# Performance work log

Measured on AMD Instinct MI355X. Metric: run time of the kernel, lower is better.

The kernel has to match this reference:

```python
import jax, jax.numpy as jnp
import numpy as np

N, D_IN, D_OUT = 4096, 1024, 1024
DROPOUT_RATE = 0.1


def setup_inputs() -> dict:
    key = jax.random.key(0)
    kx, kq, kk, kv = jax.random.split(key, 4)
    s = 1.0 / np.sqrt(D_IN)
    return {
        "x": jax.random.normal(kx, (N, D_IN), dtype=jnp.float32),
        "wq": jax.random.normal(kq, (D_OUT, D_IN), dtype=jnp.float32) * s,
        "wk": jax.random.normal(kk, (D_OUT, D_IN), dtype=jnp.float32) * s,
        "wv": jax.random.normal(kv, (D_OUT, D_IN), dtype=jnp.float32) * s,
    }


def reference(x, wq, wk, wv):
    # torch Linear: y = x @ W.T  (no bias since qkv_bias=False)
    q = x @ wq.T                      # [N, d_out]
    k = x @ wk.T
    v = x @ wv.T
    scores = q @ k.T                  # [N, N]
    n = scores.shape[0]
    causal = jnp.tril(jnp.ones((n, n), dtype=bool))  # keep lower triangle
    masked = jnp.where(causal, scores, -jnp.inf)
    scale = k.shape[-1] ** 0.5
    weights = jax.nn.softmax(masked / scale, axis=-1)
    # dropout (train mode), fixed key for determinism
    keep = jax.random.bernoulli(jax.random.key(42), 1.0 - DROPOUT_RATE, weights.shape)
    weights = jnp.where(keep, weights / (1.0 - DROPOUT_RATE), 0.0)
    return weights @ v                # [N, d_out]
```

## Files before the change

### kernel.cpp

```cpp
#include <hip/hip_runtime.h>
#include <hip/hip_fp16.h>

typedef __attribute__((ext_vector_type(8))) _Float16 f16x8;
typedef __attribute__((ext_vector_type(4))) float f32x4;

typedef const __attribute__((address_space(1))) void gas_void;
typedef __attribute__((address_space(3))) void las_void;
typedef __attribute__((address_space(3))) const __half las_chalf;

__device__ __forceinline__ f16x8 ldsr(const __half* p) {
    f16x8 r;
    asm volatile("ds_read_b128 %0, %1" : "=v"(r) : "v"((las_chalf*)p));
    return r;
}

__global__ __launch_bounds__(256) void cast_all_k(const float* __restrict__ x,
                                                  const float* __restrict__ wq,
                                                  const float* __restrict__ wk,
                                                  const float* __restrict__ wv,
                                                  __half* __restrict__ xb,
                                                  __half* __restrict__ wqkv) {
    const int b = blockIdx.x;
    const float* src;
    __half* dst;
    size_t i;
    if (b < 2048) {
        src = x; dst = xb;
        i = ((size_t)b * 256 + threadIdx.x) * 8;
    } else {
        const int w = (b - 2048) >> 9;
        src = w == 0 ? wq : (w == 1 ? wk : wv);
        dst = wqkv + (size_t)w * 1048576;
        i = (((size_t)((b - 2048) & 511)) * 256 + threadIdx.x) * 8;
    }
    float4 a = *(const float4*)(src + i);
    float4 c = *(const float4*)(src + i + 4);
    __half2 h[4] = { __floats2half2_rn(a.x, a.y), __floats2half2_rn(a.z, a.w),
                     __floats2half2_rn(c.x, c.y), __floats2half2_rn(c.z, c.w) };
    *(int4*)(dst + i) = *(int4*)h;
}

template <int MODE>
__global__ __launch_bounds__(512, 2)
void gemm256(const __half* __restrict__ pA, const __half* __restrict__ pB,
             void* __restrict__ pC, void* __restrict__ pC2,
             __half* __restrict__ PH1, __half* __restrict__ PH2,
             __half* __restrict__ PH3, __half* __restrict__ PH4,
             const float* __restrict__ Lr) {
    constexpr int LD = (MODE == 0) ? 1024 : (MODE == 1 ? 2048 : 4096);

    int bi, bj, c = 0, k_lo = 0, NT = 16;
    bool isVT = false;
    if constexpr (MODE == 0) {
        const int id = blockIdx.x;
        const int sw = (id & 7) * 24 + (id >> 3);
        if (sw < 128) { bi = sw >> 3; bj = sw & 7; }
        else          { int s2 = sw - 128; bi = s2 >> 4; bj = s2 & 15; isVT = true; }
    } else if constexpr (MODE == 1) {
        const int id = blockIdx.x;
        const int sw = (id & 7) * 17 + (id >> 3);
        int b = (int)((sqrtf(8.0f * sw + 1.0f) - 1.0f) * 0.5f);
        while ((b + 1) * (b + 2) / 2 <= sw) ++b;
        while (b * (b + 1) / 2 > sw) --b;
        bi = b; bj = sw - b * (b + 1) / 2;
    } else {
        const int id = blockIdx.x;
        const int xcd = id & 7;
        const int sw = (xcd < 4 ? xcd * 25 : 100 + (xcd - 4) * 24) + (id >> 3);
        bj = sw / 49;
        int x = sw - 49 * bj;
        int nch = 1;
        for (bi = 0; bi < 16; ++bi) {
            nch = (4 * (bi + 1) + 12) / 13;
            if (x < nch) { c = x; break; }
            x -= nch;
        }
        const int full = 4 * (bi + 1);
        k_lo = c * 13;
        NT = min(full - k_lo, 13);
    }

    const __half* A = pA;
    const __half* B = pB;
    if constexpr (MODE == 0) {
        if (isVT) { A = pB + 2097152; B = pA; }
    }

    const int brow = bi * 256, bcol = bj * 256;
    const int tid = threadIdx.x;
    const int lane = tid & 63, wid = tid >> 6;
    const int wm = wid >> 2, wn = wid & 3;
    const int lane15 = lane & 15;
    const int kxor = (lane & 7) << 3;
    const int g16 = (lane >> 4) << 3;

    extern __shared__ __half smem[];

    const int srow = (wid << 3) + (lane >> 3);
    const int scol = ((lane & 7) ^ ((lane >> 3) & 7)) << 3;

    auto stage_half = [&](const __half* G, int growbase, int kt, int buf, int mat, int half) {
        const __half* src = G + (size_t)(growbase + half * 128 + srow) * LD + kt * 64 + scol;
        __half* dst = &smem[buf * 32768 + mat * 16384 + (half * 128 + (wid << 3)) * 64];
        __builtin_amdgcn_global_load_lds((gas_void*)src, (las_void*)dst, 16, 0, 0);
        __builtin_amdgcn_global_load_lds((gas_void*)(src + (size_t)64 * LD),
                                         (las_void*)(dst + 64 * 64), 16, 0, 0);
    };

    f32x4 acc[8][4] = {};
    f16x8 bfrag[2][4];

    stage_half(B, bcol, k_lo, 0, 1, 0);
    stage_half(B, bcol, k_lo, 0, 1, 1);
    stage_half(A, brow, k_lo, 0, 0, 0);
    stage_half(A, brow, k_lo, 0, 0, 1);
    if (NT > 1) {
        stage_half(B, bcol, k_lo + 1, 1, 1, 0);
        stage_half(B, bcol, k_lo + 1, 1, 1, 1);
    }

    for (int Tr = 0; Tr < NT; ++Tr) {
        const int Ta = k_lo + Tr;
        const int buf = Tr & 1;
        const __half* Abase = &smem[buf * 32768 + (wm * 128 + lane15) * 64];
        const __half* Bbase = &smem[buf * 32768 + 16384 + (wn * 64 + lane15) * 64];

        if (Tr < NT - 1) asm volatile("s_waitcnt vmcnt(4)" ::: "memory");
        else             asm volatile("s_waitcnt vmcnt(0)" ::: "memory");
        __builtin_amdgcn_s_barrier();

        {
#pragma unroll
            for (int kk = 0; kk < 2; ++kk)
#pragma unroll
                for (int n = 0; n < 4; ++n)
                    bfrag[kk][n] = ldsr(Bbase + (n * 16) * 64 + ((kk * 32 + g16) ^ kxor));
            f16x8 af[2][2];
#pragma unroll
            for (int mi = 0; mi < 2; ++mi)
#pragma unroll
                for (int kk = 0; kk < 2; ++kk)
                    af[mi][kk] = ldsr(Abase + (mi * 16) * 64 + ((kk * 32 + g16) ^ kxor));
            if (Tr + 1 < NT) stage_half(A, brow, Ta + 1, buf ^ 1, 0, 0);
            asm volatile("s_waitcnt lgkmcnt(0)" ::: "memory");
            __builtin_amdgcn_sched_barrier(0);
            __builtin_amdgcn_s_setprio(1);
#pragma unroll
            for (int mi = 0; mi < 2; ++mi)
#pragma unroll
                for (int n = 0; n < 4; ++n)
#pragma unroll
                    for (int kk = 0; kk < 2; ++kk)
                        acc[mi][n] = __builtin_amdgcn_mfma_f32_16x16x32_f16(
                            af[mi][kk], bfrag[kk][n], acc[mi][n], 0, 0, 0);
            __builtin_amdgcn_s_setprio(0);
            __builtin_amdgcn_s_barrier();
        }

#pragma unroll
        for (int p = 1; p < 4; ++p) {
            f16x8 af[2][2];
#pragma unroll
            for (int mi = 0; mi < 2; ++mi)
#pragma unroll
                for (int kk = 0; kk < 2; ++kk)
                    af[mi][kk] = ldsr(Abase + ((2 * p + mi) * 16) * 64 + ((kk * 32 + g16) ^ kxor));
            if (p == 1)      { if (Tr + 1 < NT) stage_half(A, brow, Ta + 1, buf ^ 1, 0, 1); }
            else if (p == 2) { if (Tr + 2 < NT) stage_half(B, bcol, Ta + 2, buf, 1, 0); }
            else             { if (Tr + 2 < NT) stage_half(B, bcol, Ta + 2, buf, 1, 1); }
            asm volatile("s_waitcnt lgkmcnt(0)" ::: "memory");
            __builtin_amdgcn_sched_barrier(0);
            __builtin_amdgcn_s_setprio(1);
#pragma unroll
            for (int mi = 0; mi < 2; ++mi)
#pragma unroll
                for (int n = 0; n < 4; ++n)
#pragma unroll
                    for (int kk = 0; kk < 2; ++kk)
                        acc[2 * p + mi][n] = __builtin_amdgcn_mfma_f32_16x16x32_f16(
                            af[mi][kk], bfrag[kk][n], acc[2 * p + mi][n], 0, 0, 0);
            __builtin_amdgcn_s_setprio(0);
            __builtin_amdgcn_s_barrier();
        }
    }

    const int r0 = (lane >> 4) << 2;
    if constexpr (MODE == 2) {
        if (c == 0) {
            float* Ct = (float*)pC;
            const bool doScale = (4 * (bi + 1) <= 13);
#pragma unroll
            for (int m = 0; m < 8; ++m)
#pragma unroll
                for (int r = 0; r < 4; ++r) {
                    const int row = brow + wm * 128 + m * 16 + r0 + r;
                    const float inv = doScale ? 1.0f / (0.9f * Lr[row]) : 1.0f;
#pragma unroll
                    for (int n = 0; n < 4; ++n) {
                        const int col = bcol + wn * 64 + n * 16 + lane15;
                        Ct[(size_t)row * 1024 + col] = acc[m][n][r] * inv;
                    }
                }
        } else {
            __half* Ph = (c == 1) ? PH1 : (c == 2 ? PH2 : (c == 3 ? PH3 : PH4));
#pragma unroll
            for (int m = 0; m < 8; ++m)
#pragma unroll
                for (int n = 0; n < 4; ++n) {
                    const int col = bcol + wn * 64 + n * 16 + lane15;
#pragma unroll
                    for (int r = 0; r < 4; ++r) {
                        const int row = brow + wm * 128 + m * 16 + r0 + r;
                        Ph[(size_t)row * 1024 + col] = __float2half(acc[m][n][r]);
                    }
                }
        }
    } else {
        __half* Ct = (__half*)pC;
        int ldc = (MODE == 1) ? 4096 : 2048;
        const float scl = (MODE == 1) ? 0.03125f : 1.0f;
        if constexpr (MODE == 0) {
            if (isVT) { Ct = (__half*)pC2; ldc = 4096; }
        }
#pragma unroll
        for (int m = 0; m < 8; ++m)
#pragma unroll
            for (int n = 0; n < 4; ++n) {
                const int col = bcol + wn * 64 + n * 16 + lane15;
#pragma unroll
                for (int r = 0; r < 4; ++r) {
                    const int row = brow + wm * 128 + m * 16 + r0 + r;
                    Ct[(size_t)row * ldc + col] = __float2half(acc[m][n][r] * scl);
                }
            }
    }
}

__global__ __launch_bounds__(256) void pv_merge_k(float* __restrict__ out,
                                                  const __half* __restrict__ PH1,
                                                  const __half* __restrict__ PH2,
                                                  const __half* __restrict__ PH3,
                                                  const __half* __restrict__ PH4,
                                                  const float* __restrict__ L) {
    const int row = 768 + blockIdx.x;
    const int bi = row >> 8;
    const int nch = (4 * (bi + 1) + 12) / 13;
    const float inv = 1.0f / (0.9f * L[row]);
    const size_t o = (size_t)row * 1024 + threadIdx.x * 4;
    float4 s = *(float4*)(out + o);
    const __half* planes[4] = { PH1, PH2, PH3, PH4 };
#pragma unroll 4
    for (int cc = 1; cc < nch; ++cc) {
        const __half2* p2 = (const __half2*)(planes[cc - 1] + o);
        float2 a = __half22float2(p2[0]);
        float2 b = __half22float2(p2[1]);
        s.x += a.x; s.y += a.y; s.z += b.x; s.w += b.y;
    }
    s.x *= inv; s.y *= inv; s.z *= inv; s.w *= inv;
    *(float4*)(out + o) = s;
}

__device__ __forceinline__ uint32_t rotl32(uint32_t x, int d) { return (x << d) | (x >> (32 - d)); }

__device__ __forceinline__ bool keep_bit(uint32_t flat) {
    uint32_t x0 = 0u;
    uint32_t x1 = flat;
    const uint32_t ks0 = 0u, ks1 = 42u, ks2 = 0u ^ 42u ^ 0x1BD11BDAu;
    x0 += ks0; x1 += ks1;
#define TFR(r) { x0 += x1; x1 = rotl32(x1, r); x1 ^= x0; }
    TFR(13) TFR(15) TFR(26) TFR(6)   x0 += ks1; x1 += ks2 + 1u;
    TFR(17) TFR(29) TFR(16) TFR(24)  x0 += ks2; x1 += ks0 + 2u;
    TFR(13) TFR(15) TFR(26) TFR(6)   x0 += ks0; x1 += ks1 + 3u;
    TFR(17) TFR(29) TFR(16) TFR(24)  x0 += ks1; x1 += ks2 + 4u;
    TFR(13) TFR(15) TFR(26) TFR(6)   x0 += ks2; x1 += ks0 + 5u;
#undef TFR
    uint32_t bits = x0 ^ x1;
    float u = __uint_as_float((bits >> 9) | 0x3f800000u) - 1.0f;
    return u < 0.9f;
}

__global__ __launch_bounds__(256) void softdrop_k(__half* __restrict__ SP,
                                                  float* __restrict__ L, int N) {
    const int i = blockIdx.x;
    const int tid = threadIdx.x;
    const int len = i + 1;
    __half* row = SP + (size_t)i * N;

    float l = 0.f;
    const int len8 = len & ~7;
    for (int j = tid * 8; j < len8; j += 2048) {
        int4 pk = *(const int4*)(row + j);
        const __half* hp = (const __half*)&pk;
        __half o8[8];
        const uint32_t base = (uint32_t)i * 4096u + (uint32_t)j;
#pragma unroll
        for (int q = 0; q < 8; ++q) {
            float e = __expf(__half2float(hp[q]));
            l += e;
            o8[q] = keep_bit(base + q) ? __float2half(e) : __float2half(0.0f);
        }
        *(int4*)(row + j) = *(int4*)o8;
    }
    for (int j = len8 + tid; j < len; j += 256) {
        float e = __expf(__half2float(row[j]));
        l += e;
        row[j] = keep_bit((uint32_t)i * 4096u + (uint32_t)j) ? __float2half(e) : __float2half(0.0f);
    }

    for (int off = 1; off < 64; off <<= 1) l += __shfl_xor(l, off);
    __shared__ float ls[4];
    if ((tid & 63) == 0) ls[tid >> 6] = l;
    __syncthreads();
    if (tid == 0) L[i] = ls[0] + ls[1] + ls[2] + ls[3];

    const int zlim = ((i >> 8) << 8) + 256;
    const int za = (len + 7) & ~7;
    for (int j = len + tid; j < min(za, zlim); j += 256) row[j] = __float2half(0.0f);
    const int4 z = {0, 0, 0, 0};
    for (int j = za + tid * 8; j < zlim; j += 2048) *(int4*)(row + j) = z;
}

extern "C" void kernel_launch(void* const* d_in, const int* in_sizes, int n_in,
                              void* d_out, int out_size, void* d_ws, size_t ws_size,
                              hipStream_t stream) {
    const float* x  = (const float*)d_in[0];
    const float* wq = (const float*)d_in[1];
    const float* wk = (const float*)d_in[2];
    const float* wv = (const float*)d_in[3];
    float* out = (float*)d_out;
    char* ws = (char*)d_ws;

    const int N = 4096;

    __half* xb   = (__half*)(ws + 0);
    __half* wqkv = (__half*)(ws + 8388608);
    __half* QK   = (__half*)(ws + 14680064);
    __half* VT   = (__half*)(ws + 31457280);
    __half* SP   = (__half*)(ws + 48234496);
    float*  Lr   = (float*)(ws + 81788928);
    __half* PH1  = (__half*)(ws + 83886080);
    __half* PH2  = (__half*)(ws + 92274688);
    __half* PH3  = (__half*)(ws + 100663296);
    __half* PH4  = (__half*)(ws + 109051904);

    __half* Q = QK;
    __half* K = QK + 1024;

    auto* g0 = gemm256<0>;
    auto* g1 = gemm256<1>;
    auto* g2 = gemm256<2>;
    (void)hipFuncSetAttribute((const void*)g0, hipFuncAttributeMaxDynamicSharedMemorySize, 131072);
    (void)hipFuncSetAttribute((const void*)g1, hipFuncAttributeMaxDynamicSharedMemorySize, 131072);
    (void)hipFuncSetAttribute((const void*)g2, hipFuncAttributeMaxDynamicSharedMemorySize, 131072);

    cast_all_k<<<3584, 256, 0, stream>>>(x, wq, wk, wv, xb, wqkv);

    g0<<<192, 512, 131072, stream>>>(xb, wqkv, QK, VT, nullptr, nullptr, nullptr, nullptr, nullptr);

    g1<<<136, 512, 131072, stream>>>(Q, K, SP, nullptr, nullptr, nullptr, nullptr, nullptr, nullptr);

    softdrop_k<<<N, 256, 0, stream>>>(SP, Lr, N);

    g2<<<196, 512, 131072, stream>>>(SP, VT, out, nullptr, PH1, PH2, PH3, PH4, Lr);

    pv_merge_k<<<3328, 256, 0, stream>>>(out, PH1, PH2, PH3, PH4, Lr);
}
```

Measured before the change: 139.3 us.

## Precompute dropout bitmask in idle QK^T GEMM blocks and zero diagonal in epilogue

```diff
diff --git a/kernel.cpp b/kernel.cpp
--- a/kernel.cpp
+++ b/kernel.cpp
@@ -12,6 +12,25 @@
     f16x8 r;
     asm volatile("ds_read_b128 %0, %1" : "=v"(r) : "v"((las_chalf*)p));
     return r;
+}
+
+__device__ __forceinline__ uint32_t rotl32(uint32_t x, int d) { return (x << d) | (x >> (32 - d)); }
+
+__device__ __forceinline__ bool keep_bit(uint32_t flat) {
+    uint32_t x0 = 0u;
+    uint32_t x1 = flat;
+    const uint32_t ks0 = 0u, ks1 = 42u, ks2 = 0u ^ 42u ^ 0x1BD11BDAu;
+    x0 += ks0; x1 += ks1;
+#define TFR(r) { x0 += x1; x1 = rotl32(x1, r); x1 ^= x0; }
+    TFR(13) TFR(15) TFR(26) TFR(6)   x0 += ks1; x1 += ks2 + 1u;
+    TFR(17) TFR(29) TFR(16) TFR(24)  x0 += ks2; x1 += ks0 + 2u;
+    TFR(13) TFR(15) TFR(26) TFR(6)   x0 += ks0; x1 += ks1 + 3u;
+    TFR(17) TFR(29) TFR(16) TFR(24)  x0 += ks1; x1 += ks2 + 4u;
+    TFR(13) TFR(15) TFR(26) TFR(6)   x0 += ks2; x1 += ks0 + 5u;
+#undef TFR
+    uint32_t bits = x0 ^ x1;
+    float u = __uint_as_float((bits >> 9) | 0x3f800000u) - 1.0f;
+    return u < 0.9f;
 }
 
 __global__ __launch_bounds__(256) void cast_all_k(const float* __restrict__ x,
@@ -46,8 +65,10 @@
              void* __restrict__ pC, void* __restrict__ pC2,
              __half* __restrict__ PH1, __half* __restrict__ PH2,
              __half* __restrict__ PH3, __half* __restrict__ PH4,
-             const float* __restrict__ Lr) {
+             const float* __restrict__ Lr, unsigned char* __restrict__ mask) {
     constexpr int LD = (MODE == 0) ? 1024 : (MODE == 1 ? 2048 : 4096);
+
+    const int tid = threadIdx.x;
 
     int bi, bj, c = 0, k_lo = 0, NT = 16;
     bool isVT = false;
@@ -58,6 +79,28 @@
         else          { int s2 = sw - 128; bi = s2 >> 4; bj = s2 & 15; isVT = true; }
     } else if constexpr (MODE == 1) {
         const int id = blockIdx.x;
+        if (id >= 136) {
+            const int mid = id - 136;
+            for (int pr = mid; pr < 2048; pr += 120) {
+                const int ra = pr;
+                const int rb = 4095 - pr;
+                const int nba = (ra >> 3) + 1;
+                const int nbb = (rb >> 3) + 1;
+                const int tot = nba + nbb;
+                for (int t = tid; t < tot; t += 512) {
+                    int row, b0;
+                    if (t < nba) { row = ra; b0 = t << 3; }
+                    else         { row = rb; b0 = (t - nba) << 3; }
+                    const uint32_t base = (uint32_t)row * 4096u + (uint32_t)b0;
+                    uint32_t bits = 0;
+#pragma unroll
+                    for (int q = 0; q < 8; ++q)
+                        bits |= (keep_bit(base + q) ? 1u : 0u) << q;
+                    mask[(size_t)row * 512 + (b0 >> 3)] = (unsigned char)bits;
+                }
+            }
+            return;
+        }
         const int sw = (id & 7) * 17 + (id >> 3);
         int b = (int)((sqrtf(8.0f * sw + 1.0f) - 1.0f) * 0.5f);
         while ((b + 1) * (b + 2) / 2 <= sw) ++b;
@@ -87,7 +130,6 @@
     }
 
     const int brow = bi * 256, bcol = bj * 256;
-    const int tid = threadIdx.x;
     const int lane = tid & 63, wid = tid >> 6;
     const int wm = wid >> 2, wn = wid & 3;
     const int lane15 = lane & 15;
@@ -222,6 +264,7 @@
         if constexpr (MODE == 0) {
             if (isVT) { Ct = (__half*)pC2; ldc = 4096; }
         }
+        const bool dz = (MODE == 1) && (bi == bj);
 #pragma unroll
         for (int m = 0; m < 8; ++m)
 #pragma unroll
@@ -230,7 +273,9 @@
 #pragma unroll
                 for (int r = 0; r < 4; ++r) {
                     const int row = brow + wm * 128 + m * 16 + r0 + r;
-                    Ct[(size_t)row * ldc + col] = __float2half(acc[m][n][r] * scl);
+                    float v = acc[m][n][r] * scl;
+                    if (dz && col > row) v = 0.0f;
+                    Ct[(size_t)row * ldc + col] = __float2half(v);
                 }
             }
     }
@@ -260,51 +305,35 @@
     *(float4*)(out + o) = s;
 }
 
-__device__ __forceinline__ uint32_t rotl32(uint32_t x, int d) { return (x << d) | (x >> (32 - d)); }
-
-__device__ __forceinline__ bool keep_bit(uint32_t flat) {
-    uint32_t x0 = 0u;
-    uint32_t x1 = flat;
-    const uint32_t ks0 = 0u, ks1 = 42u, ks2 = 0u ^ 42u ^ 0x1BD11BDAu;
-    x0 += ks0; x1 += ks1;
-#define TFR(r) { x0 += x1; x1 = rotl32(x1, r); x1 ^= x0; }
-    TFR(13) TFR(15) TFR(26) TFR(6)   x0 += ks1; x1 += ks2 + 1u;
-    TFR(17) TFR(29) TFR(16) TFR(24)  x0 += ks2; x1 += ks0 + 2u;
-    TFR(13) TFR(15) TFR(26) TFR(6)   x0 += ks0; x1 += ks1 + 3u;
-    TFR(17) TFR(29) TFR(16) TFR(24)  x0 += ks1; x1 += ks2 + 4u;
-    TFR(13) TFR(15) TFR(26) TFR(6)   x0 += ks2; x1 += ks0 + 5u;
-#undef TFR
-    uint32_t bits = x0 ^ x1;
-    float u = __uint_as_float((bits >> 9) | 0x3f800000u) - 1.0f;
-    return u < 0.9f;
-}
-
 __global__ __launch_bounds__(256) void softdrop_k(__half* __restrict__ SP,
-                                                  float* __restrict__ L, int N) {
+                                                  float* __restrict__ L,
+                                                  const unsigned char* __restrict__ mask,
+                                                  int N) {
     const int i = blockIdx.x;
     const int tid = threadIdx.x;
     const int len = i + 1;
     __half* row = SP + (size_t)i * N;
+    const unsigned char* mrow = mask + (size_t)i * 512;
 
     float l = 0.f;
     const int len8 = len & ~7;
     for (int j = tid * 8; j < len8; j += 2048) {
         int4 pk = *(const int4*)(row + j);
         const __half* hp = (const __half*)&pk;
+        const unsigned int mb = mrow[j >> 3];
         __half o8[8];
-        const uint32_t base = (uint32_t)i * 4096u + (uint32_t)j;
 #pragma unroll
         for (int q = 0; q < 8; ++q) {
             float e = __expf(__half2float(hp[q]));
             l += e;
-            o8[q] = keep_bit(base + q) ? __float2half(e) : __float2half(0.0f);
+            o8[q] = ((mb >> q) & 1u) ? __float2half(e) : __float2half(0.0f);
         }
         *(int4*)(row + j) = *(int4*)o8;
     }
     for (int j = len8 + tid; j < len; j += 256) {
         float e = __expf(__half2float(row[j]));
         l += e;
-        row[j] = keep_bit((uint32_t)i * 4096u + (uint32_t)j) ? __float2half(e) : __float2half(0.0f);
+        row[j] = ((mrow[j >> 3] >> (j & 7)) & 1u) ? __float2half(e) : __float2half(0.0f);
     }
 
     for (int off = 1; off < 64; off <<= 1) l += __shfl_xor(l, off);
@@ -312,12 +341,6 @@
     if ((tid & 63) == 0) ls[tid >> 6] = l;
     __syncthreads();
     if (tid == 0) L[i] = ls[0] + ls[1] + ls[2] + ls[3];
-
-    const int zlim = ((i >> 8) << 8) + 256;
-    const int za = (len + 7) & ~7;
-    for (int j = len + tid; j < min(za, zlim); j += 256) row[j] = __float2half(0.0f);
-    const int4 z = {0, 0, 0, 0};
-    for (int j = za + tid * 8; j < zlim; j += 2048) *(int4*)(row + j) = z;
 }
 
 extern "C" void kernel_launch(void* const* d_in, const int* in_sizes, int n_in,
@@ -342,6 +365,7 @@
     __half* PH2  = (__half*)(ws + 92274688);
     __half* PH3  = (__half*)(ws + 100663296);
     __half* PH4  = (__half*)(ws + 109051904);
+    unsigned char* mask8 = (unsigned char*)(ws + 117440512);
 
     __half* Q = QK;
     __half* K = QK + 1024;
@@ -355,13 +379,15 @@
 
     cast_all_k<<<3584, 256, 0, stream>>>(x, wq, wk, wv, xb, wqkv);
 
-    g0<<<192, 512, 131072, stream>>>(xb, wqkv, QK, VT, nullptr, nullptr, nullptr, nullptr, nullptr);
-
-    g1<<<136, 512, 131072, stream>>>(Q, K, SP, nullptr, nullptr, nullptr, nullptr, nullptr, nullptr);
-
-    softdrop_k<<<N, 256, 0, stream>>>(SP, Lr, N);
-
-    g2<<<196, 512, 131072, stream>>>(SP, VT, out, nullptr, PH1, PH2, PH3, PH4, Lr);
+    g0<<<192, 512, 131072, stream>>>(xb, wqkv, QK, VT, nullptr, nullptr, nullptr, nullptr,
+                                     nullptr, nullptr);
+
+    g1<<<256, 512, 131072, stream>>>(Q, K, SP, nullptr, nullptr, nullptr, nullptr, nullptr,
+                                     nullptr, mask8);
+
+    softdrop_k<<<N, 256, 0, stream>>>(SP, Lr, mask8, N);
+
+    g2<<<196, 512, 131072, stream>>>(SP, VT, out, nullptr, PH1, PH2, PH3, PH4, Lr, nullptr);
 
     pv_merge_k<<<3328, 256, 0, stream>>>(out, PH1, PH2, PH3, PH4, Lr);
 }
```

After: 175.5 us. +26.0%, slower.
